# Kernel optimization log

Hardware: AMD Instinct MI355X
Metric: run time of the kernel (lower is better)

The kernel has to match this reference:

```python
import jax, jax.numpy as jnp
import numpy as np

B, SEQ, DIM = 2, 2048, 1024
H = 16
DH = DIM // H            # 64, head dim; LayerNorm is over this axis
LAT = 512
CTX = SEQ - LAT          # 1536
SCALE = DH ** -0.5
LN_EPS = 1e-5


def _rotary_cos_sin(n):
    # lucidrains RotaryEmbedding: inv_freq = 1/10000^(2i/d); emb = cat(freqs, freqs)
    inv_freq = 1.0 / (10000.0 ** (jnp.arange(0, DH, 2, dtype=jnp.float32) / DH))
    freqs = jnp.arange(n, dtype=jnp.float32)[:, None] * inv_freq[None, :]
    emb = jnp.concatenate([freqs, freqs], axis=-1)  # [n, DH]
    return jnp.cos(emb), jnp.sin(emb)


def _rotate_half(t):
    t1, t2 = jnp.split(t, 2, axis=-1)
    return jnp.concatenate([-t2, t1], axis=-1)


def _layernorm(t, g, b):
    m = jnp.mean(t, axis=-1, keepdims=True)
    v = jnp.var(t, axis=-1, keepdims=True)
    return (t - m) / jnp.sqrt(v + LN_EPS) * g + b


def setup_inputs() -> dict:
    key = jax.random.key(0)
    ks = jax.random.split(key, 4)
    x = jax.random.normal(ks[0], (B, SEQ, DIM), dtype=jnp.float32)
    Wq = jax.random.normal(ks[1], (DIM, DIM), dtype=jnp.float32) * 0.02
    Wkv = jax.random.normal(ks[2], (DIM, DIM), dtype=jnp.float32) * 0.02
    Wo = jax.random.normal(ks[3], (DIM, DIM), dtype=jnp.float32) * 0.02
    bo = jnp.zeros((DIM,), dtype=jnp.float32)
    ln_g = jnp.ones((DH,), dtype=jnp.float32)
    ln_b = jnp.zeros((DH,), dtype=jnp.float32)
    return {"x": x, "Wq": Wq, "Wkv": Wkv, "Wo": Wo, "bo": bo, "ln_g": ln_g, "ln_b": ln_b}


def reference(x, Wq, Wkv, Wo, bo, ln_g, ln_b):
    b, n, d = x.shape
    neg = -jnp.finfo(x.dtype).max

    # projections (torch Linear: y = x @ W.T)
    q = x @ Wq.T
    kv = x @ Wkv.T

    def split_heads(t):  # b n (h d) -> (b h) n d
        return t.reshape(b, n, H, DH).transpose(0, 2, 1, 3).reshape(b * H, n, DH)

    q = split_heads(q)
    kv = split_heads(kv)

    cos, sin = _rotary_cos_sin(n)  # [n, DH], broadcasts over (b h)
    q = q * cos + _rotate_half(q) * sin
    kv = kv * cos + _rotate_half(kv) * sin

    q_lat = q[:, CTX:] * SCALE   # [(bh), LAT, DH]
    q_ctx = q[:, :CTX] * SCALE   # [(bh), CTX, DH]

    lkv = _layernorm(kv, ln_g, ln_b)       # key layernorm over head dim
    lkv_ctx = lkv[:, :CTX]                 # per-position LN => slice equals norm(kv_ctx)

    # latent branch: latent queries over full sequence, causal only on latent block
    lsim = jnp.einsum('bid,bjd->bij', q_lat, lkv)  # [(bh), LAT, n]
    lat = n - CTX
    causal = jnp.triu(jnp.ones((lat, lat), dtype=bool), 1)
    mask = jnp.concatenate([jnp.zeros((lat, CTX), dtype=bool), causal], axis=-1)
    lsim = jnp.where(mask, neg, lsim)
    attn = jax.nn.softmax(lsim, axis=-1)
    out = jnp.einsum('bij,bjd->bid', attn, lkv)    # [(bh), LAT, DH]

    # context branch: context queries over context keys, NO causal mask
    lsim_ctx = jnp.einsum('bid,bjd->bij', q_ctx, lkv_ctx)
    attn_ctx = jax.nn.softmax(lsim_ctx, axis=-1)
    out_ctx = jnp.einsum('bij,bjd->bid', attn_ctx, lkv_ctx)  # [(bh), CTX, DH]

    def merge_heads(t):  # (b h) m d -> b m (h d)
        m = t.shape[1]
        return t.reshape(b, H, m, DH).transpose(0, 2, 1, 3).reshape(b, m, H * DH)

    # original concatenates latent output FIRST, then context
    out_all = jnp.concatenate([merge_heads(out), merge_heads(out_ctx)], axis=1)
    return out_all @ Wo.T + bo
```

## Files before the change

kernel.cpp:

```cpp
#include <hip/hip_runtime.h>
#include <cstdint>
#include <cstddef>

typedef unsigned short u16;
typedef __bf16 bf16x8 __attribute__((ext_vector_type(8)));
typedef __bf16 bf16x2 __attribute__((ext_vector_type(2)));
typedef float f32x4 __attribute__((ext_vector_type(4)));
typedef float f32x16 __attribute__((ext_vector_type(16)));

#define DEV __device__ __forceinline__

DEV float bf2f(u16 v) { union { unsigned u; float f; } x; x.u = ((unsigned)v) << 16; return x.f; }
DEV u16 f2bf(float f) {
  union { float f; unsigned u; } x; x.f = f;
  unsigned u = x.u + 0x7fffu + ((x.u >> 16) & 1u);
  return (u16)(u >> 16);
}

DEV float fexp2(float x) {
#if __has_builtin(__builtin_amdgcn_exp2f)
  return __builtin_amdgcn_exp2f(x);
#else
  return exp2f(x);
#endif
}

DEV f32x4 mfma16(bf16x8 a, bf16x8 b, f32x4 c) {
  return __builtin_amdgcn_mfma_f32_16x16x32_bf16(a, b, c, 0, 0, 0);
}
DEV f32x16 mfma32(bf16x8 a, bf16x8 b, f32x16 c) {
  return __builtin_amdgcn_mfma_f32_32x32x16_bf16(a, b, c, 0, 0, 0);
}

DEV void stage16(const void* g, void* l) {
#if __has_builtin(__builtin_amdgcn_global_load_lds)
  __builtin_amdgcn_global_load_lds((__attribute__((address_space(1))) void*)g,
                                   (__attribute__((address_space(3))) void*)l, 16, 0, 0);
#else
  *(uint4*)l = *(const uint4*)g;
#endif
}

DEV unsigned pkbf(float a, float b) {
  bf16x2 v = {(__bf16)a, (__bf16)b};
  return __builtin_bit_cast(unsigned, v);
}

DEV void plswap(unsigned& a, unsigned& b) {
#if __has_builtin(__builtin_amdgcn_permlane32_swap)
  auto r = __builtin_amdgcn_permlane32_swap(a, b, false, false);
  a = (unsigned)r[0];
  b = (unsigned)r[1];
#else
  unsigned sa = __shfl_xor((int)a, 32), sb = __shfl_xor((int)b, 32);
  bool hi = ((threadIdx.x & 63) >> 5) != 0;
  unsigned na = hi ? sb : a;
  unsigned nb = hi ? b : sa;
  a = na; b = nb;
#endif
}

DEV void xcd_square(int lin, int& mt, int& nt) {
  const int x = lin & 7, i = lin >> 3;
  mt = ((x & 3) << 3) | (i >> 3);
  nt = ((x >> 2) << 3) | (i & 7);
}

__global__ __launch_bounds__(256) void cvt_all(const float* __restrict__ x,
                                               const float* __restrict__ Wq,
                                               const float* __restrict__ Wkv,
                                               const float* __restrict__ Wo,
                                               u16* __restrict__ xb,
                                               u16* __restrict__ wqkv,
                                               u16* __restrict__ wo,
                                               float2* __restrict__ tab) {
  const int blk = blockIdx.x;
  if (blk >= 7168) {
    const int idx = (blk - 7168) * 256 + threadIdx.x;
    const int pos = idx >> 5, fi = idx & 31;
    float ang = (float)pos * exp2f((float)fi * -0.415241011860919f);
    float sn, cs;
    sincosf(ang, &sn, &cs);
    tab[idx] = make_float2(cs, sn);
    return;
  }
  const float* src; u16* dst; int base;
  if (blk < 4096)      { src = x;   dst = xb;             base = blk; }
  else if (blk < 5120) { src = Wq;  dst = wqkv;           base = blk - 4096; }
  else if (blk < 6144) { src = Wkv; dst = wqkv + 1048576; base = blk - 5120; }
  else                 { src = Wo;  dst = wo;             base = blk - 6144; }
  const int i = (base * 256 + threadIdx.x) * 4;
  float4 v = *(const float4*)(src + i);
  ushort4 o;
  o.x = f2bf(v.x); o.y = f2bf(v.y); o.z = f2bf(v.z); o.w = f2bf(v.w);
  *(ushort4*)(dst + i) = o;
}

__global__ __launch_bounds__(256) void gemm_qkv(const u16* __restrict__ A,
                                                const u16* __restrict__ Bm,
                                                const float2* __restrict__ tab,
                                                const float* __restrict__ lng,
                                                const float* __restrict__ lnb,
                                                u16* __restrict__ q_b,
                                                u16* __restrict__ k_b,
                                                u16* __restrict__ vT_b) {
  __shared__ u16 As[2][8192];
  __shared__ u16 Bs[2][8192];
  const int tid = threadIdx.x;
  const int lane = tid & 63;
  const int lo = lane & 15, hi = lane >> 4;
  const int wid = tid >> 6;
  const int wr = wid >> 1, wc = wid & 1;
  int mt, nt;
  xcd_square(blockIdx.y * 16 + blockIdx.x, mt, nt);
  const long m0 = (long)mt * 128;
  const long n0 = (long)nt * 128;

  f32x4 acc[4][4];
  const f32x4 vzero = {0.f, 0.f, 0.f, 0.f};
#pragma unroll
  for (int i = 0; i < 4; ++i)
#pragma unroll
    for (int j = 0; j < 4; ++j) acc[i][j] = vzero;

  const char* Abase = (const char*)(A + m0 * 1024);
  const char* Bbase = (const char*)(Bm + n0 * 1024);

#pragma unroll
  for (int i = 0; i < 4; ++i) {
    int o = (i * 256 + tid) * 16;
    int row = o >> 7, kb = o & 127;
    int sc = kb ^ ((row & 7) << 4);
    stage16(Abase + (long)row * 2048 + sc, (char*)As[0] + o);
    stage16(Bbase + (long)row * 2048 + sc, (char*)Bs[0] + o);
  }

  int cur = 0;
  for (int kt = 0; kt < 16; ++kt) {
    if (kt + 1 < 16) {
      const int kb0 = (kt + 1) * 128;
#pragma unroll
      for (int i = 0; i < 4; ++i) {
        int o = (i * 256 + tid) * 16;
        int row = o >> 7, kb = o & 127;
        int sc = kb ^ ((row & 7) << 4);
        stage16(Abase + (long)row * 2048 + kb0 + sc, (char*)As[cur ^ 1] + o);
        stage16(Bbase + (long)row * 2048 + kb0 + sc, (char*)Bs[cur ^ 1] + o);
      }
      asm volatile("s_waitcnt vmcnt(8)" ::: "memory");
    } else {
      asm volatile("s_waitcnt vmcnt(0)" ::: "memory");
    }
    __builtin_amdgcn_s_barrier();
    __builtin_amdgcn_sched_barrier(0);
#pragma unroll
    for (int ks = 0; ks < 2; ++ks) {
      bf16x8 af[4], bfr[4];
#pragma unroll
      for (int mi = 0; mi < 4; ++mi) {
        const int row = wr * 64 + mi * 16 + lo;
        af[mi] = *(const bf16x8*)((const char*)As[cur] +
                                  ((row * 128 + ks * 64 + hi * 16) ^ ((row & 7) << 4)));
      }
#pragma unroll
      for (int ni = 0; ni < 4; ++ni) {
        const int row = wc * 64 + ni * 16 + lo;
        bfr[ni] = *(const bf16x8*)((const char*)Bs[cur] +
                                   ((row * 128 + ks * 64 + hi * 16) ^ ((row & 7) << 4)));
      }
#pragma unroll
      for (int mi = 0; mi < 4; ++mi)
#pragma unroll
        for (int ni = 0; ni < 4; ++ni)
          acc[mi][ni] = mfma16(af[mi], bfr[ni], acc[mi][ni]);
    }
    __builtin_amdgcn_sched_barrier(0);
    __builtin_amdgcn_s_barrier();
    cur ^= 1;
  }

  const int brow = (int)(m0 >> 11);
  const bool isQ = (n0 < 1024);
  const int hbase = isQ ? (int)(n0 >> 6) : (int)((n0 - 1024) >> 6);
  const int h = hbase + wc;
  const int bh = brow * 16 + h;
  float lg[4], lb[4];
  if (!isQ) {
#pragma unroll
    for (int ni = 0; ni < 4; ++ni) {
      lg[ni] = lng[ni * 16 + lo];
      lb[ni] = lnb[ni * 16 + lo];
    }
  }
#pragma unroll
  for (int mi = 0; mi < 4; ++mi) {
    const int pos0 = ((int)m0 & 2047) + wr * 64 + mi * 16 + hi * 4;
    float cs[2][4], sn[2][4];
#pragma unroll
    for (int p = 0; p < 2; ++p)
#pragma unroll
      for (int r = 0; r < 4; ++r) {
        float2 t = tab[(pos0 + r) * 32 + p * 16 + lo];
        cs[p][r] = t.x; sn[p][r] = t.y;
      }
    float o[4][4];
#pragma unroll
    for (int ni = 0; ni < 4; ++ni) {
      const float sgn = (ni < 2) ? -1.f : 1.f;
#pragma unroll
      for (int r = 0; r < 4; ++r)
        o[ni][r] = acc[mi][ni][r] * cs[ni & 1][r] + sgn * acc[mi][ni ^ 2][r] * sn[ni & 1][r];
    }
    if (isQ) {
#pragma unroll
      for (int ni = 0; ni < 4; ++ni)
#pragma unroll
        for (int r = 0; r < 4; ++r)
          q_b[((size_t)bh * 2048 + pos0 + r) * 64 + ni * 16 + lo] =
              f2bf(o[ni][r] * 0.18033688f);
    } else {
      float s1[4], s2[4];
#pragma unroll
      for (int r = 0; r < 4; ++r) {
        s1[r] = o[0][r] + o[1][r] + o[2][r] + o[3][r];
        s2[r] = o[0][r] * o[0][r] + o[1][r] * o[1][r] + o[2][r] * o[2][r] + o[3][r] * o[3][r];
      }
#pragma unroll
      for (int msk = 1; msk < 16; msk <<= 1)
#pragma unroll
        for (int r = 0; r < 4; ++r) {
          s1[r] += __shfl_xor(s1[r], msk);
          s2[r] += __shfl_xor(s2[r], msk);
        }
      u16 kv16[4][4];
#pragma unroll
      for (int r = 0; r < 4; ++r) {
        const float mean = s1[r] * (1.f / 64.f);
        const float var = s2[r] * (1.f / 64.f) - mean * mean;
        const float rstd = rsqrtf(var + 1e-5f);
#pragma unroll
        for (int ni = 0; ni < 4; ++ni) {
          const float lk = (o[ni][r] - mean) * rstd * lg[ni] + lb[ni];
          kv16[ni][r] = f2bf(lk);
          k_b[((size_t)bh * 2048 + pos0 + r) * 64 + ni * 16 + lo] = kv16[ni][r];
        }
      }
#pragma unroll
      for (int ni = 0; ni < 4; ++ni) {
        ushort4 w4 = {kv16[ni][0], kv16[ni][1], kv16[ni][2], kv16[ni][3]};
        *(ushort4*)&vT_b[((size_t)bh * 64 + ni * 16 + lo) * 2048 + pos0] = w4;
      }
    }
  }
}

__global__ __launch_bounds__(256) void gemm_out(const u16* __restrict__ A,
                                                const u16* __restrict__ Bm,
                                                float* __restrict__ Cf,
                                                const float* __restrict__ bias) {
  __shared__ u16 As[2][8192];
  __shared__ u16 Bs[2][4096];
  const int tid = threadIdx.x;
  const int lane = tid & 63;
  const int lo = lane & 15, hi = lane >> 4;
  const int wid = tid >> 6;
  const int wr = wid >> 1, wc = wid & 1;
  int mt, nt;
  xcd_square(blockIdx.y * 16 + blockIdx.x, mt, nt);
  const long m0 = (long)mt * 128;
  const long n0 = (long)nt * 64;

  f32x4 acc[4][2];
  const f32x4 vzero = {0.f, 0.f, 0.f, 0.f};
#pragma unroll
  for (int i = 0; i < 4; ++i) {
    acc[i][0] = vzero; acc[i][1] = vzero;
  }

  const char* Abase = (const char*)(A + m0 * 1024);
  const char* Bbase = (const char*)(Bm + n0 * 1024);

#pragma unroll
  for (int i = 0; i < 4; ++i) {
    int o = (i * 256 + tid) * 16;
    int row = o >> 7, kb = o & 127;
    int sc = kb ^ ((row & 7) << 4);
    stage16(Abase + (long)row * 2048 + sc, (char*)As[0] + o);
  }
#pragma unroll
  for (int i = 0; i < 2; ++i) {
    int o = (i * 256 + tid) * 16;
    int row = o >> 7, kb = o & 127;
    int sc = kb ^ ((row & 7) << 4);
    stage16(Bbase + (long)row * 2048 + sc, (char*)Bs[0] + o);
  }

  int cur = 0;
  for (int kt = 0; kt < 16; ++kt) {
    if (kt + 1 < 16) {
      const int kb0 = (kt + 1) * 128;
#pragma unroll
      for (int i = 0; i < 4; ++i) {
        int o = (i * 256 + tid) * 16;
        int row = o >> 7, kb = o & 127;
        int sc = kb ^ ((row & 7) << 4);
        stage16(Abase + (long)row * 2048 + kb0 + sc, (char*)As[cur ^ 1] + o);
      }
#pragma unroll
      for (int i = 0; i < 2; ++i) {
        int o = (i * 256 + tid) * 16;
        int row = o >> 7, kb = o & 127;
        int sc = kb ^ ((row & 7) << 4);
        stage16(Bbase + (long)row * 2048 + kb0 + sc, (char*)Bs[cur ^ 1] + o);
      }
      asm volatile("s_waitcnt vmcnt(6)" ::: "memory");
    } else {
      asm volatile("s_waitcnt vmcnt(0)" ::: "memory");
    }
    __builtin_amdgcn_s_barrier();
    __builtin_amdgcn_sched_barrier(0);
#pragma unroll
    for (int ks = 0; ks < 2; ++ks) {
      bf16x8 af[4], bfr[2];
#pragma unroll
      for (int mi = 0; mi < 4; ++mi) {
        const int row = wr * 64 + mi * 16 + lo;
        af[mi] = *(const bf16x8*)((const char*)As[cur] +
                                  ((row * 128 + ks * 64 + hi * 16) ^ ((row & 7) << 4)));
      }
#pragma unroll
      for (int ni = 0; ni < 2; ++ni) {
        const int row = wc * 32 + ni * 16 + lo;
        bfr[ni] = *(const bf16x8*)((const char*)Bs[cur] +
                                   ((row * 128 + ks * 64 + hi * 16) ^ ((row & 7) << 4)));
      }
#pragma unroll
      for (int mi = 0; mi < 4; ++mi)
#pragma unroll
        for (int ni = 0; ni < 2; ++ni)
          acc[mi][ni] = mfma16(af[mi], bfr[ni], acc[mi][ni]);
    }
    __builtin_amdgcn_sched_barrier(0);
    __builtin_amdgcn_s_barrier();
    cur ^= 1;
  }
#pragma unroll
  for (int mi = 0; mi < 4; ++mi)
#pragma unroll
    for (int ni = 0; ni < 2; ++ni) {
      const long col = n0 + wc * 32 + ni * 16 + lo;
      const float bs = bias[col];
#pragma unroll
      for (int r = 0; r < 4; ++r) {
        const long row = m0 + wr * 64 + mi * 16 + hi * 4 + r;
        Cf[row * 1024 + col] = acc[mi][ni][r] + bs;
      }
    }
}

__global__ __launch_bounds__(256, 2) void attn_kernel(const u16* __restrict__ q_b,
                                                      const u16* __restrict__ k_b,
                                                      const u16* __restrict__ vT_b,
                                                      u16* __restrict__ out_all) {
  __shared__ __align__(16) char smem[65536];
  __shared__ float ldsLs[2][2][32];
  __shared__ float ldsLi[2][2][32];
  const int tid = threadIdx.x;
  const int wid = tid >> 6, lane = tid & 63;
  const int l31 = lane & 31, lh = lane >> 5;
  const int half = wid >> 1, wp = wid & 1;
  const int bid = blockIdx.x;
  const int xcd = bid & 7, rest = bid >> 3;
  const int bh = (xcd << 2) | (rest & 3);
  const int unit = rest >> 2;
  const int b = bh >> 4, h = bh & 15;
  const bool lat = unit >= 12;
  const int q0b = lat ? 1536 + (unit - 12) * 128 : unit * 128;
  const int q0w = q0b + wp * 64;
  const int nkt_tot = lat ? ((q0b + 128) >> 6) : 24;
  const int nhalf = nkt_tot >> 1;
  const int kt0 = half * nhalf;
  const int wave_kmax = lat ? (q0w + 63) : 1535;
  const char* kg = (const char*)(k_b + (size_t)bh * 2048 * 64);
  const char* vg = (const char*)(vT_b + (size_t)bh * 64 * 2048);
  char* Kbuf0 = smem + half * 32768;
  char* Kbuf1 = Kbuf0 + 8192;
  char* Vbuf0 = Kbuf0 + 16384;
  char* Vbuf1 = Kbuf0 + 24576;
  const f32x16 vzero16 = {0.f,0.f,0.f,0.f,0.f,0.f,0.f,0.f,0.f,0.f,0.f,0.f,0.f,0.f,0.f,0.f};

  bf16x8 qf[2][4];
#pragma unroll
  for (int s = 0; s < 2; ++s) {
    const u16* qrow = q_b + ((size_t)bh * 2048 + q0w + s * 32 + l31) * 64;
#pragma unroll
    for (int ds = 0; ds < 4; ++ds)
      qf[s][ds] = *(const bf16x8*)(qrow + ds * 16 + lh * 8);
  }

  float lsum[2] = {0.f, 0.f};
  f32x16 oacc[2][2];
  oacc[0][0] = vzero16; oacc[0][1] = vzero16;
  oacc[1][0] = vzero16; oacc[1][1] = vzero16;

  const int t127 = tid & 127;

  {
    const int kb0 = kt0 << 6;
#pragma unroll
    for (int i = 0; i < 4; ++i) {
      const int off = t127 * 16 + i * 2048;
      const int row = off >> 7, colb = off & 127;
      const int sc = colb ^ ((row & 7) << 4);
      stage16(kg + (size_t)(kb0 + row) * 128 + sc, Kbuf0 + off);
      stage16(vg + (size_t)row * 4096 + (size_t)(kb0 << 1) + sc, Vbuf0 + off);
    }
  }

  for (int t = 0; t < nhalf; ++t) {
    const int kt = kt0 + t;
    const int k0 = kt << 6;
    const bool more = (t + 1 < nhalf);
    const char* Kc = (t & 1) ? Kbuf1 : Kbuf0;
    const char* Vc = (t & 1) ? Vbuf1 : Vbuf0;
    char* Kn = (t & 1) ? Kbuf0 : Kbuf1;
    char* Vn = (t & 1) ? Vbuf0 : Vbuf1;
    if (more) {
      const int k0n = k0 + 64;
#pragma unroll
      for (int i = 0; i < 4; ++i) {
        const int off = t127 * 16 + i * 2048;
        const int row = off >> 7, colb = off & 127;
        const int sc = colb ^ ((row & 7) << 4);
        stage16(kg + (size_t)(k0n + row) * 128 + sc, Kn + off);
        stage16(vg + (size_t)row * 4096 + (size_t)(k0n << 1) + sc, Vn + off);
      }
      asm volatile("s_waitcnt vmcnt(8)" ::: "memory");
    } else {
      asm volatile("s_waitcnt vmcnt(0)" ::: "memory");
    }
    __builtin_amdgcn_s_barrier();
    __builtin_amdgcn_sched_barrier(0);
    if (k0 <= wave_kmax) {
      const int sw = (l31 & 7) << 4;
      bf16x8 kfr[2][4];
      bf16x8 bv[4][2];
#pragma unroll
      for (int kb = 0; kb < 2; ++kb) {
        const char* kr = Kc + (kb * 32 + l31) * 128;
#pragma unroll
        for (int ds = 0; ds < 4; ++ds)
          kfr[kb][ds] = *(const bf16x8*)(kr + ((ds * 32 + lh * 16) ^ sw));
      }
#pragma unroll
      for (int db = 0; db < 2; ++db) {
        const char* vr = Vc + (db * 32 + l31) * 128;
#pragma unroll
        for (int t4 = 0; t4 < 4; ++t4)
          bv[t4][db] = *(const bf16x8*)(vr + ((t4 * 32 + lh * 16) ^ sw));
      }
      f32x16 s32[2][2];
      __builtin_amdgcn_s_setprio(1);
#pragma unroll
      for (int kb = 0; kb < 2; ++kb)
#pragma unroll
        for (int s = 0; s < 2; ++s) {
          f32x16 acc = vzero16;
#pragma unroll
          for (int ds = 0; ds < 4; ++ds)
            acc = mfma32(kfr[kb][ds], qf[s][ds], acc);
          s32[s][kb] = acc;
        }
      __builtin_amdgcn_s_setprio(0);
      unsigned w[2][16];
#pragma unroll
      for (int s = 0; s < 2; ++s) {
        if (lat && (k0 + 63 > q0w + s * 32)) {
          const int qg = q0w + s * 32 + l31;
#pragma unroll
          for (int kb = 0; kb < 2; ++kb)
#pragma unroll
            for (int r = 0; r < 16; ++r) {
              const int key = k0 + kb * 32 + (r & 3) + 8 * (r >> 2) + 4 * lh;
              if (key > qg) s32[s][kb][r] = -1e30f;
            }
        }
#pragma unroll
        for (int kb = 0; kb < 2; ++kb) {
          float p[16];
#pragma unroll
          for (int r = 0; r < 16; ++r) {
            p[r] = fexp2(s32[s][kb][r]);
            lsum[s] += p[r];
          }
#pragma unroll
          for (int m = 0; m < 8; ++m) w[s][kb * 8 + m] = pkbf(p[2 * m], p[2 * m + 1]);
        }
      }
#pragma unroll
      for (int t4 = 0; t4 < 4; ++t4) {
        const int g = t4 * 4;
        union { unsigned uw[4]; bf16x8 v; } A[2];
#pragma unroll
        for (int s = 0; s < 2; ++s) {
          plswap(w[s][g], w[s][g + 2]);
          plswap(w[s][g + 1], w[s][g + 3]);
          A[s].uw[0] = w[s][g];     A[s].uw[1] = w[s][g + 1];
          A[s].uw[2] = w[s][g + 2]; A[s].uw[3] = w[s][g + 3];
        }
        __builtin_amdgcn_s_setprio(1);
#pragma unroll
        for (int db = 0; db < 2; ++db) {
          oacc[0][db] = mfma32(A[0].v, bv[t4][db], oacc[0][db]);
          oacc[1][db] = mfma32(A[1].v, bv[t4][db], oacc[1][db]);
        }
        __builtin_amdgcn_s_setprio(0);
      }
    }
    __builtin_amdgcn_sched_barrier(0);
    __builtin_amdgcn_s_barrier();
  }

  float* mergeO = (float*)smem + (size_t)wp * 4096;
  if (half == 1) {
#pragma unroll
    for (int s = 0; s < 2; ++s) {
      float ls = lsum[s] + __shfl_xor(lsum[s], 32);
      if (lh == 0) ldsLs[wp][s][l31] = ls;
#pragma unroll
      for (int db = 0; db < 2; ++db)
#pragma unroll
        for (int r = 0; r < 16; ++r) {
          const int qv = (r & 3) + 8 * (r >> 2) + 4 * lh;
          mergeO[(s * 32 + qv) * 64 + db * 32 + l31] = oacc[s][db][r];
        }
    }
  }
  __syncthreads();
  if (half == 0) {
#pragma unroll
    for (int s = 0; s < 2; ++s) {
      float ls = lsum[s] + __shfl_xor(lsum[s], 32) + ldsLs[wp][s][l31];
      if (lh == 0) ldsLi[wp][s][l31] = 1.f / ls;
    }
    const int orow0 = lat ? (q0w - 1536) : (512 + q0w);
#pragma unroll
    for (int s = 0; s < 2; ++s)
#pragma unroll
      for (int db = 0; db < 2; ++db)
#pragma unroll
        for (int r = 0; r < 16; ++r) {
          const int qv = (r & 3) + 8 * (r >> 2) + 4 * lh;
          const float o = oacc[s][db][r] + mergeO[(s * 32 + qv) * 64 + db * 32 + l31];
          out_all[((size_t)b * 2048 + orow0 + s * 32 + qv) * 1024 + h * 64 + db * 32 + l31] =
              f2bf(o * ldsLi[wp][s][qv]);
        }
  }
}

extern "C" void kernel_launch(void* const* d_in, const int* in_sizes, int n_in,
                              void* d_out, int out_size, void* d_ws, size_t ws_size,
                              hipStream_t stream) {
  const float* x    = (const float*)d_in[0];
  const float* Wq   = (const float*)d_in[1];
  const float* Wkv  = (const float*)d_in[2];
  const float* Wo   = (const float*)d_in[3];
  const float* bo   = (const float*)d_in[4];
  const float* ln_g = (const float*)d_in[5];
  const float* ln_b = (const float*)d_in[6];
  float* out = (float*)d_out;
  char* ws = (char*)d_ws;

  u16*    xb      = (u16*)(ws + 0);
  u16*    out_all = (u16*)(ws + 0);
  u16*    wqkv_b  = (u16*)(ws + (size_t)(8u << 20));
  u16*    wo_b    = (u16*)(ws + (size_t)(12u << 20));
  float2* tab     = (float2*)(ws + (size_t)(14u << 20));
  u16*    q_b     = (u16*)(ws + (size_t)(15u << 20));
  u16*    k_b     = (u16*)(ws + (size_t)(23u << 20));
  u16*    vT_b    = (u16*)(ws + (size_t)(31u << 20));

  cvt_all<<<7424, 256, 0, stream>>>(x, Wq, Wkv, Wo, xb, wqkv_b, wo_b, tab);
  gemm_qkv<<<dim3(16, 32), 256, 0, stream>>>(xb, wqkv_b, tab, ln_g, ln_b,
                                             q_b, k_b, vT_b);
  attn_kernel<<<512, 256, 0, stream>>>(q_b, k_b, vT_b, out_all);
  gemm_out<<<dim3(16, 32), 256, 0, stream>>>(out_all, wo_b, out, bo);
}
```

Before: 101.8 us.

## Enlarge GEMM tiles: 256x128 QKV tiles with 512 threads, 128x128 output tiles

```diff
diff --git a/kernel.cpp b/kernel.cpp
--- a/kernel.cpp
+++ b/kernel.cpp
@@ -58,12 +58,6 @@
   unsigned nb = hi ? b : sa;
   a = na; b = nb;
 #endif
-}
-
-DEV void xcd_square(int lin, int& mt, int& nt) {
-  const int x = lin & 7, i = lin >> 3;
-  mt = ((x & 3) << 3) | (i >> 3);
-  nt = ((x >> 2) << 3) | (i & 7);
 }
 
 __global__ __launch_bounds__(256) void cvt_all(const float* __restrict__ x,
@@ -96,7 +90,7 @@
   *(ushort4*)(dst + i) = o;
 }
 
-__global__ __launch_bounds__(256) void gemm_qkv(const u16* __restrict__ A,
+__global__ __launch_bounds__(512) void gemm_qkv(const u16* __restrict__ A,
                                                 const u16* __restrict__ Bm,
                                                 const float2* __restrict__ tab,
                                                 const float* __restrict__ lng,
@@ -104,6 +98,173 @@
                                                 u16* __restrict__ q_b,
                                                 u16* __restrict__ k_b,
                                                 u16* __restrict__ vT_b) {
+  __shared__ u16 As[2][16384];
+  __shared__ u16 Bs[2][8192];
+  const int tid = threadIdx.x;
+  const int lane = tid & 63;
+  const int lo = lane & 15, hi = lane >> 4;
+  const int wid = tid >> 6;
+  const int wr = wid >> 1, wc = wid & 1;
+  const int lin = blockIdx.x;
+  const int xx = lin & 7, ii = lin >> 3;
+  const int mt = ((xx & 3) << 2) | (ii >> 3);
+  const int nt = ((xx >> 2) << 3) | (ii & 7);
+  const long m0 = (long)mt * 256;
+  const long n0 = (long)nt * 128;
+
+  f32x4 acc[4][4];
+  const f32x4 vzero = {0.f, 0.f, 0.f, 0.f};
+#pragma unroll
+  for (int i = 0; i < 4; ++i)
+#pragma unroll
+    for (int j = 0; j < 4; ++j) acc[i][j] = vzero;
+
+  const char* Abase = (const char*)(A + m0 * 1024);
+  const char* Bbase = (const char*)(Bm + n0 * 1024);
+
+#pragma unroll
+  for (int i = 0; i < 4; ++i) {
+    int o = (i * 512 + tid) * 16;
+    int row = o >> 7, kb = o & 127;
+    int sc = kb ^ ((row & 7) << 4);
+    stage16(Abase + (long)row * 2048 + sc, (char*)As[0] + o);
+  }
+#pragma unroll
+  for (int i = 0; i < 2; ++i) {
+    int o = (i * 512 + tid) * 16;
+    int row = o >> 7, kb = o & 127;
+    int sc = kb ^ ((row & 7) << 4);
+    stage16(Bbase + (long)row * 2048 + sc, (char*)Bs[0] + o);
+  }
+
+  int cur = 0;
+  for (int kt = 0; kt < 16; ++kt) {
+    if (kt + 1 < 16) {
+      const int kb0 = (kt + 1) * 128;
+#pragma unroll
+      for (int i = 0; i < 4; ++i) {
+        int o = (i * 512 + tid) * 16;
+        int row = o >> 7, kb = o & 127;
+        int sc = kb ^ ((row & 7) << 4);
+        stage16(Abase + (long)row * 2048 + kb0 + sc, (char*)As[cur ^ 1] + o);
+      }
+#pragma unroll
+      for (int i = 0; i < 2; ++i) {
+        int o = (i * 512 + tid) * 16;
+        int row = o >> 7, kb = o & 127;
+        int sc = kb ^ ((row & 7) << 4);
+        stage16(Bbase + (long)row * 2048 + kb0 + sc, (char*)Bs[cur ^ 1] + o);
+      }
+      asm volatile("s_waitcnt vmcnt(6)" ::: "memory");
+    } else {
+      asm volatile("s_waitcnt vmcnt(0)" ::: "memory");
+    }
+    __builtin_amdgcn_s_barrier();
+    __builtin_amdgcn_sched_barrier(0);
+#pragma unroll
+    for (int ks = 0; ks < 2; ++ks) {
+      bf16x8 af[4], bfr[4];
+#pragma unroll
+      for (int mi = 0; mi < 4; ++mi) {
+        const int row = wr * 64 + mi * 16 + lo;
+        af[mi] = *(const bf16x8*)((const char*)As[cur] +
+                                  ((row * 128 + ks * 64 + hi * 16) ^ ((row & 7) << 4)));
+      }
+#pragma unroll
+      for (int ni = 0; ni < 4; ++ni) {
+        const int row = wc * 64 + ni * 16 + lo;
+        bfr[ni] = *(const bf16x8*)((const char*)Bs[cur] +
+                                   ((row * 128 + ks * 64 + hi * 16) ^ ((row & 7) << 4)));
+      }
+#pragma unroll
+      for (int mi = 0; mi < 4; ++mi)
+#pragma unroll
+        for (int ni = 0; ni < 4; ++ni)
+          acc[mi][ni] = mfma16(af[mi], bfr[ni], acc[mi][ni]);
+    }
+    __builtin_amdgcn_sched_barrier(0);
+    __builtin_amdgcn_s_barrier();
+    cur ^= 1;
+  }
+
+  const int brow = mt >> 3;
+  const bool isQ = (nt < 8);
+  const int h = (isQ ? nt * 2 : (nt - 8) * 2) + wc;
+  const int bh = brow * 16 + h;
+  float lg[4], lb[4];
+  if (!isQ) {
+#pragma unroll
+    for (int ni = 0; ni < 4; ++ni) {
+      lg[ni] = lng[ni * 16 + lo];
+      lb[ni] = lnb[ni * 16 + lo];
+    }
+  }
+#pragma unroll
+  for (int mi = 0; mi < 4; ++mi) {
+    const int pos0 = (mt & 7) * 256 + wr * 64 + mi * 16 + hi * 4;
+    float cs[2][4], sn[2][4];
+#pragma unroll
+    for (int p = 0; p < 2; ++p)
+#pragma unroll
+      for (int r = 0; r < 4; ++r) {
+        float2 t = tab[(pos0 + r) * 32 + p * 16 + lo];
+        cs[p][r] = t.x; sn[p][r] = t.y;
+      }
+    float o[4][4];
+#pragma unroll
+    for (int ni = 0; ni < 4; ++ni) {
+      const float sgn = (ni < 2) ? -1.f : 1.f;
+#pragma unroll
+      for (int r = 0; r < 4; ++r)
+        o[ni][r] = acc[mi][ni][r] * cs[ni & 1][r] + sgn * acc[mi][ni ^ 2][r] * sn[ni & 1][r];
+    }
+    if (isQ) {
+#pragma unroll
+      for (int ni = 0; ni < 4; ++ni)
+#pragma unroll
+        for (int r = 0; r < 4; ++r)
+          q_b[((size_t)bh * 2048 + pos0 + r) * 64 + ni * 16 + lo] =
+              f2bf(o[ni][r] * 0.18033688f);
+    } else {
+      float s1[4], s2[4];
+#pragma unroll
+      for (int r = 0; r < 4; ++r) {
+        s1[r] = o[0][r] + o[1][r] + o[2][r] + o[3][r];
+        s2[r] = o[0][r] * o[0][r] + o[1][r] * o[1][r] + o[2][r] * o[2][r] + o[3][r] * o[3][r];
+      }
+#pragma unroll
+      for (int msk = 1; msk < 16; msk <<= 1)
+#pragma unroll
+        for (int r = 0; r < 4; ++r) {
+          s1[r] += __shfl_xor(s1[r], msk);
+          s2[r] += __shfl_xor(s2[r], msk);
+        }
+      u16 kv16[4][4];
+#pragma unroll
+      for (int r = 0; r < 4; ++r) {
+        const float mean = s1[r] * (1.f / 64.f);
+        const float var = s2[r] * (1.f / 64.f) - mean * mean;
+        const float rstd = rsqrtf(var + 1e-5f);
+#pragma unroll
+        for (int ni = 0; ni < 4; ++ni) {
+          const float lk = (o[ni][r] - mean) * rstd * lg[ni] + lb[ni];
+          kv16[ni][r] = f2bf(lk);
+          k_b[((size_t)bh * 2048 + pos0 + r) * 64 + ni * 16 + lo] = kv16[ni][r];
+        }
+      }
+#pragma unroll
+      for (int ni = 0; ni < 4; ++ni) {
+        ushort4 w4 = {kv16[ni][0], kv16[ni][1], kv16[ni][2], kv16[ni][3]};
+        *(ushort4*)&vT_b[((size_t)bh * 64 + ni * 16 + lo) * 2048 + pos0] = w4;
+      }
+    }
+  }
+}
+
+__global__ __launch_bounds__(256) void gemm_out(const u16* __restrict__ A,
+                                                const u16* __restrict__ Bm,
+                                                float* __restrict__ Cf,
+                                                const float* __restrict__ bias) {
   __shared__ u16 As[2][8192];
   __shared__ u16 Bs[2][8192];
   const int tid = threadIdx.x;
@@ -111,8 +272,10 @@
   const int lo = lane & 15, hi = lane >> 4;
   const int wid = tid >> 6;
   const int wr = wid >> 1, wc = wid & 1;
-  int mt, nt;
-  xcd_square(blockIdx.y * 16 + blockIdx.x, mt, nt);
+  const int lin = blockIdx.x;
+  const int xx = lin & 7, ii = lin >> 3;
+  const int mt = ((xx & 3) << 3) | (ii >> 2);
+  const int nt = ((xx >> 2) << 2) | (ii & 3);
   const long m0 = (long)mt * 128;
   const long n0 = (long)nt * 128;
 
@@ -178,177 +341,11 @@
     __builtin_amdgcn_s_barrier();
     cur ^= 1;
   }
-
-  const int brow = (int)(m0 >> 11);
-  const bool isQ = (n0 < 1024);
-  const int hbase = isQ ? (int)(n0 >> 6) : (int)((n0 - 1024) >> 6);
-  const int h = hbase + wc;
-  const int bh = brow * 16 + h;
-  float lg[4], lb[4];
-  if (!isQ) {
+#pragma unroll
+  for (int mi = 0; mi < 4; ++mi)
 #pragma unroll
     for (int ni = 0; ni < 4; ++ni) {
-      lg[ni] = lng[ni * 16 + lo];
-      lb[ni] = lnb[ni * 16 + lo];
-    }
-  }
-#pragma unroll
-  for (int mi = 0; mi < 4; ++mi) {
-    const int pos0 = ((int)m0 & 2047) + wr * 64 + mi * 16 + hi * 4;
-    float cs[2][4], sn[2][4];
-#pragma unroll
-    for (int p = 0; p < 2; ++p)
-#pragma unroll
-      for (int r = 0; r < 4; ++r) {
-        float2 t = tab[(pos0 + r) * 32 + p * 16 + lo];
-        cs[p][r] = t.x; sn[p][r] = t.y;
-      }
-    float o[4][4];
-#pragma unroll
-    for (int ni = 0; ni < 4; ++ni) {
-      const float sgn = (ni < 2) ? -1.f : 1.f;
-#pragma unroll
-      for (int r = 0; r < 4; ++r)
-        o[ni][r] = acc[mi][ni][r] * cs[ni & 1][r] + sgn * acc[mi][ni ^ 2][r] * sn[ni & 1][r];
-    }
-    if (isQ) {
-#pragma unroll
-      for (int ni = 0; ni < 4; ++ni)
-#pragma unroll
-        for (int r = 0; r < 4; ++r)
-          q_b[((size_t)bh * 2048 + pos0 + r) * 64 + ni * 16 + lo] =
-              f2bf(o[ni][r] * 0.18033688f);
-    } else {
-      float s1[4], s2[4];
-#pragma unroll
-      for (int r = 0; r < 4; ++r) {
-        s1[r] = o[0][r] + o[1][r] + o[2][r] + o[3][r];
-        s2[r] = o[0][r] * o[0][r] + o[1][r] * o[1][r] + o[2][r] * o[2][r] + o[3][r] * o[3][r];
-      }
-#pragma unroll
-      for (int msk = 1; msk < 16; msk <<= 1)
-#pragma unroll
-        for (int r = 0; r < 4; ++r) {
-          s1[r] += __shfl_xor(s1[r], msk);
-          s2[r] += __shfl_xor(s2[r], msk);
-        }
-      u16 kv16[4][4];
-#pragma unroll
-      for (int r = 0; r < 4; ++r) {
-        const float mean = s1[r] * (1.f / 64.f);
-        const float var = s2[r] * (1.f / 64.f) - mean * mean;
-        const float rstd = rsqrtf(var + 1e-5f);
-#pragma unroll
-        for (int ni = 0; ni < 4; ++ni) {
-          const float lk = (o[ni][r] - mean) * rstd * lg[ni] + lb[ni];
-          kv16[ni][r] = f2bf(lk);
-          k_b[((size_t)bh * 2048 + pos0 + r) * 64 + ni * 16 + lo] = kv16[ni][r];
-        }
-      }
-#pragma unroll
-      for (int ni = 0; ni < 4; ++ni) {
-        ushort4 w4 = {kv16[ni][0], kv16[ni][1], kv16[ni][2], kv16[ni][3]};
-        *(ushort4*)&vT_b[((size_t)bh * 64 + ni * 16 + lo) * 2048 + pos0] = w4;
-      }
-    }
-  }
-}
-
-__global__ __launch_bounds__(256) void gemm_out(const u16* __restrict__ A,
-                                                const u16* __restrict__ Bm,
-                                                float* __restrict__ Cf,
-                                                const float* __restrict__ bias) {
-  __shared__ u16 As[2][8192];
-  __shared__ u16 Bs[2][4096];
-  const int tid = threadIdx.x;
-  const int lane = tid & 63;
-  const int lo = lane & 15, hi = lane >> 4;
-  const int wid = tid >> 6;
-  const int wr = wid >> 1, wc = wid & 1;
-  int mt, nt;
-  xcd_square(blockIdx.y * 16 + blockIdx.x, mt, nt);
-  const long m0 = (long)mt * 128;
-  const long n0 = (long)nt * 64;
-
-  f32x4 acc[4][2];
-  const f32x4 vzero = {0.f, 0.f, 0.f, 0.f};
-#pragma unroll
-  for (int i = 0; i < 4; ++i) {
-    acc[i][0] = vzero; acc[i][1] = vzero;
-  }
-
-  const char* Abase = (const char*)(A + m0 * 1024);
-  const char* Bbase = (const char*)(Bm + n0 * 1024);
-
-#pragma unroll
-  for (int i = 0; i < 4; ++i) {
-    int o = (i * 256 + tid) * 16;
-    int row = o >> 7, kb = o & 127;
-    int sc = kb ^ ((row & 7) << 4);
-    stage16(Abase + (long)row * 2048 + sc, (char*)As[0] + o);
-  }
-#pragma unroll
-  for (int i = 0; i < 2; ++i) {
-    int o = (i * 256 + tid) * 16;
-    int row = o >> 7, kb = o & 127;
-    int sc = kb ^ ((row & 7) << 4);
-    stage16(Bbase + (long)row * 2048 + sc, (char*)Bs[0] + o);
-  }
-
-  int cur = 0;
-  for (int kt = 0; kt < 16; ++kt) {
-    if (kt + 1 < 16) {
-      const int kb0 = (kt + 1) * 128;
-#pragma unroll
-      for (int i = 0; i < 4; ++i) {
-        int o = (i * 256 + tid) * 16;
-        int row = o >> 7, kb = o & 127;
-        int sc = kb ^ ((row & 7) << 4);
-        stage16(Abase + (long)row * 2048 + kb0 + sc, (char*)As[cur ^ 1] + o);
-      }
-#pragma unroll
-      for (int i = 0; i < 2; ++i) {
-        int o = (i * 256 + tid) * 16;
-        int row = o >> 7, kb = o & 127;
-        int sc = kb ^ ((row & 7) << 4);
-        stage16(Bbase + (long)row * 2048 + kb0 + sc, (char*)Bs[cur ^ 1] + o);
-      }
-      asm volatile("s_waitcnt vmcnt(6)" ::: "memory");
-    } else {
-      asm volatile("s_waitcnt vmcnt(0)" ::: "memory");
-    }
-    __builtin_amdgcn_s_barrier();
-    __builtin_amdgcn_sched_barrier(0);
-#pragma unroll
-    for (int ks = 0; ks < 2; ++ks) {
-      bf16x8 af[4], bfr[2];
-#pragma unroll
-      for (int mi = 0; mi < 4; ++mi) {
-        const int row = wr * 64 + mi * 16 + lo;
-        af[mi] = *(const bf16x8*)((const char*)As[cur] +
-                                  ((row * 128 + ks * 64 + hi * 16) ^ ((row & 7) << 4)));
-      }
-#pragma unroll
-      for (int ni = 0; ni < 2; ++ni) {
-        const int row = wc * 32 + ni * 16 + lo;
-        bfr[ni] = *(const bf16x8*)((const char*)Bs[cur] +
-                                   ((row * 128 + ks * 64 + hi * 16) ^ ((row & 7) << 4)));
-      }
-#pragma unroll
-      for (int mi = 0; mi < 4; ++mi)
-#pragma unroll
-        for (int ni = 0; ni < 2; ++ni)
-          acc[mi][ni] = mfma16(af[mi], bfr[ni], acc[mi][ni]);
-    }
-    __builtin_amdgcn_sched_barrier(0);
-    __builtin_amdgcn_s_barrier();
-    cur ^= 1;
-  }
-#pragma unroll
-  for (int mi = 0; mi < 4; ++mi)
-#pragma unroll
-    for (int ni = 0; ni < 2; ++ni) {
-      const long col = n0 + wc * 32 + ni * 16 + lo;
+      const long col = n0 + wc * 64 + ni * 16 + lo;
       const float bs = bias[col];
 #pragma unroll
       for (int r = 0; r < 4; ++r) {
@@ -581,8 +578,8 @@
   u16*    vT_b    = (u16*)(ws + (size_t)(31u << 20));
 
   cvt_all<<<7424, 256, 0, stream>>>(x, Wq, Wkv, Wo, xb, wqkv_b, wo_b, tab);
-  gemm_qkv<<<dim3(16, 32), 256, 0, stream>>>(xb, wqkv_b, tab, ln_g, ln_b,
-                                             q_b, k_b, vT_b);
+  gemm_qkv<<<256, 512, 0, stream>>>(xb, wqkv_b, tab, ln_g, ln_b,
+                                    q_b, k_b, vT_b);
   attn_kernel<<<512, 256, 0, stream>>>(q_b, k_b, vT_b, out_all);
-  gemm_out<<<dim3(16, 32), 256, 0, stream>>>(out_all, wo_b, out, bo);
-}
+  gemm_out<<<256, 256, 0, stream>>>(out_all, wo_b, out, bo);
+}
```

Result: slower. 105.0 us (+3.1%).
